# Optimization experiments

Measured on AMD Instinct MI355X. Metric: run time of the kernel, lower is better.

Reference implementation:

```python
import jax, jax.numpy as jnp
import numpy as np

NYRS = 8192
PI = np.pi
MMAX, MMIN = 0.76, 0.01
ALPH, M_TH, MU_TH = 0.093, 4.886, 5.8
ROOTD = 1000.0
I0, IF = 1, 12
M0 = 0.2

NDAYS = np.array([0, 31, 28, 31, 30, 31, 30, 31, 31, 30, 31, 30, 31], dtype=np.float64)
CDAYS = np.cumsum(NDAYS).astype(np.int64)


def _insolation_factors(phi):
    """Static (numpy) day-length factors L[12] and insolation response gE[12].
    phi is a non-differentiated scalar latitude in degrees."""
    latr = phi * PI / 180.0
    jday = np.arange(1, 366, dtype=np.float64)
    sd = np.arcsin(np.sin(PI * 23.5 / 180.0) * np.sin(PI * (jday - 80.0) / 180.0))
    y = np.clip(-np.tan(latr) * np.tan(sd), -1.0, 1.0)
    hdl = np.arccos(y)
    dtsi = hdl * np.sin(latr) * np.sin(sd) + np.cos(latr) * np.cos(sd) * np.sin(hdl)
    ndl = dtsi / dtsi.max()
    jday_mid = CDAYS[:-1] + 0.5 * NDAYS[1:]
    m_star = np.clip(1.0 - np.tan(latr) * np.tan(23.439 * PI / 180.0 * np.cos(jday_mid * PI / 182.625)), 0.0, 2.0)
    nhrs = 24.0 * np.arccos(1.0 - m_star) / PI
    L = NDAYS[1:] / 30.0 * (nhrs / 12.0)  # (12,)
    gE = np.array([ndl[CDAYS[t]:CDAYS[t + 1]].mean() for t in range(12)])  # (12,)
    return L.astype(np.float32), gE.astype(np.float32)


def setup_inputs() -> dict:
    key = jax.random.key(0)
    kT, kP = jax.random.split(key)
    T = 10.0 + 8.0 * jax.random.normal(kT, (NYRS, 12), dtype=jnp.float32)   # degC
    P = 100.0 * jax.random.uniform(kP, (NYRS, 12), dtype=jnp.float32)       # mm/month
    return {
        "syear": 0,
        "eyear": NYRS - 1,
        "phi": 45,
        "T": T,
        "P": P,
        "T1": jnp.float32(8.0),
        "T2": jnp.float32(23.0),
        "M1": jnp.float32(0.01),
        "M2": jnp.float32(0.05),
    }


def reference(syear, eyear, phi, T, P, T1, T2, M1, M2):
    nyrs = eyear - syear + 1
    L_np, gE_np = _insolation_factors(float(phi))
    L = jnp.asarray(L_np)        # (12,)
    gE = jnp.asarray(gE_np)      # (12,)

    Tm = T.T                     # (12, nyrs), month-major like torch code
    Pm = P.T                     # (12, nyrs)

    # ---- potential evapotranspiration (Thornthwaite), vectorized over all months ----
    istar = jnp.maximum(Tm / 5.0, 0.0)
    I = jnp.sum(istar ** 1.514, axis=0)                                   # (nyrs,) heat index
    a = 6.75e-07 * I ** 3 - 7.71e-05 * I ** 2 + 0.0179 * I + 0.49         # (nyrs,)
    Tsafe = jnp.clip(Tm, 0.0, 26.5)                                       # avoid neg-base pow
    Ep_mid = 16.0 * L[:, None] * (10.0 * Tsafe / I[None, :]) ** a[None, :]
    Ep_hot = -415.85 + 32.25 * Tm - 0.43 * Tm ** 2
    potEv = jnp.where(Tm < 0.0, 0.0, jnp.where(Tm < 26.5, Ep_mid, Ep_hot))  # (12, nyrs)

    # ---- leaky-bucket soil-moisture recurrence over the 12*nyrs month chain ----
    Pseq = P.reshape(-1)            # year-major month order (matches M[t,y] chain)
    Epseq = potEv.T.reshape(-1)

    def step(prevM, inp):
        p, ep = inp
        Etrans = ep * prevM * ROOTD / (MMAX * ROOTD)
        G = MU_TH * ALPH / (1.0 + MU_TH) * prevM * ROOTD
        R = p * (prevM * ROOTD / (MMAX * ROOTD)) ** M_TH + ALPH / (1.0 + MU_TH) * prevM * ROOTD
        dWdt = p - Etrans - R - G
        newM = jnp.clip(prevM + dWdt / ROOTD, MMIN, MMAX)
        return newM, newM

    _, Mseq = jax.lax.scan(step, jnp.float32(M0), (Pseq, Epseq))
    M = Mseq.reshape(nyrs, 12).T                                           # (12, nyrs)

    # ---- growth responses ----
    gT = jnp.clip((Tm - T1) / (T2 - T1), 0.0, 1.0)
    gM = jnp.clip((M - M1) / (M2 - M1), 0.0, 1.0)
    Gr = jnp.minimum(gT, gM) * gE[:, None]                                 # (12, nyrs)

    # phi > 0 and I_0 = 1 > 0  ->  width[y] = sum Gr[I0-1:IF, y]
    width = jnp.sum(Gr[I0 - 1:IF, :], axis=0)                              # (nyrs,)
    trw = (width - jnp.mean(width)) / jnp.std(width, ddof=1)               # torch.std is unbiased
    return trw
```

## Files before the change

### kernel.cpp

```cpp
#include <hip/hip_runtime.h>
#include <math.h>

#define PI_F 3.14159265358979323846f
#define WARM_Y 12
#define BY 64
#define BS 64
#define NGRP (BY + WARM_Y)
#define NPAD (NGRP * 13)

#if __has_builtin(__builtin_amdgcn_logf) && __has_builtin(__builtin_amdgcn_exp2f)
__device__ __forceinline__ float flog2(float x) { return __builtin_amdgcn_logf(x); }
__device__ __forceinline__ float fexp2(float x) { return __builtin_amdgcn_exp2f(x); }
#else
__device__ __forceinline__ float flog2(float x) { return log2f(x); }
__device__ __forceinline__ float fexp2(float x) { return exp2f(x); }
#endif
__device__ __forceinline__ float fpow(float x, float y) { return fexp2(y * flog2(x)); }

__constant__ int   c_CDAYS[13]  = {0,31,59,90,120,151,181,212,243,273,304,334,365};
__constant__ float c_NDAYSF[13] = {0,31,28,31,30,31,30,31,31,30,31,30,31};

#define POW_C 1.9345076f

__global__ void k_fused(const int* __restrict__ phi_ptr,
                        const float* __restrict__ T, const float* __restrict__ P,
                        const float* __restrict__ T1p, const float* __restrict__ T2p,
                        const float* __restrict__ M1p, const float* __restrict__ M2p,
                        float* __restrict__ width, int nyrs) {
    __shared__ float sA[NPAD];
    __shared__ float sB[NPAD];
    __shared__ float sT[NPAD];
    __shared__ float dtsi[365];
    __shared__ float sL[12], sGE[12];
    __shared__ float maxd;

    const int tid = threadIdx.x;
    const float latr = (float)(*phi_ptr) * (PI_F / 180.f);
    const float tl = tanf(latr), slat = sinf(latr), clat = cosf(latr);
    const float T1 = *T1p, T2 = *T2p, M1 = *M1p, M2 = *M2p;

    for (int d = tid; d < 365; d += BS) {
        float jd = (float)(d + 1);
        float sd = asinf(sinf(PI_F * 23.5f / 180.f) * sinf(PI_F * (jd - 80.f) / 180.f));
        float y  = fminf(1.f, fmaxf(-1.f, -tl * tanf(sd)));
        float hdl = acosf(y);
        dtsi[d] = hdl * slat * sinf(sd) + clat * cosf(sd) * sinf(hdl);
    }

    const int nmon = nyrs * 12;
    const int base = (blockIdx.x * BY - WARM_Y) * 12;
    for (int t = tid; t < NGRP * 12; t += BS) {
        int tg = base + t;
        int pt = t + t / 12;
        float p = 0.f, tt = 0.f;
        if (tg >= 0 && tg < nmon) { p = P[tg]; tt = T[tg]; }
        sB[pt] = p * 1e-3f;
        sT[pt] = tt;
    }
    __syncthreads();

    {
        float mx = -1e30f;
        for (int i = tid; i < 365; i += BS) mx = fmaxf(mx, dtsi[i]);
        for (int off = 32; off > 0; off >>= 1) mx = fmaxf(mx, __shfl_down(mx, off));
        if (tid == 0) maxd = mx;
    }
    __syncthreads();

    if (tid < 12) {
        int c0 = c_CDAYS[tid], c1 = c_CDAYS[tid + 1];
        float s = 0.f;
        for (int i = c0; i < c1; ++i) s += dtsi[i];
        sGE[tid] = (s / (float)(c1 - c0)) / maxd;
        float nd = c_NDAYSF[tid + 1];
        float jm = (float)c0 + 0.5f * nd;
        float ms = 1.f - tl * tanf(23.439f * PI_F / 180.f * cosf(jm * PI_F / 182.625f));
        ms = fminf(2.f, fmaxf(0.f, ms));
        float nhrs = 24.f * acosf(1.f - ms) / PI_F;
        sL[tid] = nd / 30.f * (nhrs / 12.f);
    }
    __syncthreads();

    for (int g = tid; g < NGRP; g += BS) {
        int yg = blockIdx.x * BY - WARM_Y + g;
        int pt = g * 13;
        if (yg < 0 || yg >= nyrs) {
#pragma unroll
            for (int m = 0; m < 12; ++m) sA[pt + m] = 1.f;
            continue;
        }
        float I = 0.f;
#pragma unroll
        for (int m = 0; m < 12; ++m) {
            float is = fmaxf(sT[pt + m] * 0.2f, 0.f);
            I += fpow(is, 1.514f);
        }
        float a  = 6.75e-07f * I * I * I - 7.71e-05f * I * I + 0.0179f * I + 0.49f;
        float rI = 10.0f / I;
#pragma unroll
        for (int m = 0; m < 12; ++m) {
            float t = sT[pt + m];
            float ep;
            if (t < 0.f)          ep = 0.f;
            else if (t < 26.5f)   ep = 16.f * sL[m] * fpow(t * rI, a);
            else                  ep = -415.85f + 32.25f * t - 0.43f * t * t;
            sA[pt + m] = (1.0f - 0.093f) - ep * (1.0f / 760.0f);
        }
    }
    __syncthreads();

    const int ly = tid;
    const int y = blockIdx.x * BY + ly;
    if (y >= nyrs) return;
    const float invT = 1.0f / (T2 - T1);
    const float invM = 1.0f / (M2 - M1);

    float M = 0.2f;
    int g0 = (blockIdx.x == 0) ? (ly < WARM_Y ? WARM_Y : ly) : ly;

    for (int g = g0; g < ly + WARM_Y; ++g) {
        int pt = g * 13;
#pragma unroll
        for (int m = 0; m < 12; ++m) {
            float a = sA[pt + m], b = sB[pt + m];
            float pw = fexp2(fmaf(4.886f, flog2(M), POW_C));
            float K = fmaf(a, M, b);
            M = fmaf(-b, pw, K);
            M = fminf(0.76f, fmaxf(0.01f, M));
        }
    }
    {
        int pt = (ly + WARM_Y) * 13;
        float acc = 0.f;
#pragma unroll
        for (int m = 0; m < 12; ++m) {
            float a = sA[pt + m], b = sB[pt + m];
            float pw = fexp2(fmaf(4.886f, flog2(M), POW_C));
            float K = fmaf(a, M, b);
            M = fmaf(-b, pw, K);
            M = fminf(0.76f, fmaxf(0.01f, M));
            float gT = fminf(fmaxf((sT[pt + m] - T1) * invT, 0.f), 1.f);
            float gM = fminf(fmaxf((M - M1) * invM, 0.f), 1.f);
            acc += fminf(gT, gM) * sGE[m];
        }
        width[y] = acc;
    }
}

__global__ void k_norm(float* __restrict__ out, int n) {
    __shared__ double s_sum[256];
    __shared__ double s_sq[256];
    __shared__ float mean_s, inv_s;
    const int t = threadIdx.x;
    double sm = 0.0, sq = 0.0;
    for (int i = t; i < n; i += 256) {
        double w = (double)out[i];
        sm += w; sq += w * w;
    }
    s_sum[t] = sm; s_sq[t] = sq;
    __syncthreads();
    for (int off = 128; off > 0; off >>= 1) {
        if (t < off) { s_sum[t] += s_sum[t + off]; s_sq[t] += s_sq[t + off]; }
        __syncthreads();
    }
    if (t == 0) {
        double mean = s_sum[0] / (double)n;
        double var = (s_sq[0] - (double)n * mean * mean) / (double)(n - 1);
        mean_s = (float)mean;
        inv_s = (float)(1.0 / sqrt(var));
    }
    __syncthreads();
    for (int i = t; i < n; i += 256) {
        out[i] = (out[i] - mean_s) * inv_s;
    }
}

extern "C" void kernel_launch(void* const* d_in, const int* in_sizes, int n_in,
                              void* d_out, int out_size, void* d_ws, size_t ws_size,
                              hipStream_t stream) {
    const int*   phi = (const int*)d_in[2];
    const float* T   = (const float*)d_in[3];
    const float* P   = (const float*)d_in[4];
    const float* T1  = (const float*)d_in[5];
    const float* T2  = (const float*)d_in[6];
    const float* M1  = (const float*)d_in[7];
    const float* M2  = (const float*)d_in[8];
    float* out = (float*)d_out;

    const int nyrs = in_sizes[3] / 12;

    k_fused<<<(nyrs + BY - 1) / BY, BS, 0, stream>>>(phi, T, P, T1, T2, M1, M2, out, nyrs);
    k_norm<<<1, 256, 0, stream>>>(out, nyrs);
}
```

Baseline: 98.18 us.

## Fuse normalization into main kernel via last-block reduction of per-block partials

Folds the separate single-block normalization kernel into the main kernel. Each block reduces its widths' sum and sum of squares in double and writes them to a workspace array. An atomic counter picks the last block, which combines the partials and normalizes the whole output. Block size rises to 256 so the setup loops (daylength table, loads) use more threads, while only 64 threads run the recurrence. It removes one kernel launch and the serial re-read of widths, but adds a memset of the counter and relies on threadfence ordering for cross-block visibility.

```diff
diff --git a/kernel.cpp b/kernel.cpp
--- a/kernel.cpp
+++ b/kernel.cpp
@@ -4,7 +4,7 @@
 #define PI_F 3.14159265358979323846f
 #define WARM_Y 12
 #define BY 64
-#define BS 64
+#define BS 256
 #define NGRP (BY + WARM_Y)
 #define NPAD (NGRP * 13)
 
@@ -22,17 +22,19 @@
 
 #define POW_C 1.9345076f
 
-__global__ void k_fused(const int* __restrict__ phi_ptr,
-                        const float* __restrict__ T, const float* __restrict__ P,
-                        const float* __restrict__ T1p, const float* __restrict__ T2p,
-                        const float* __restrict__ M1p, const float* __restrict__ M2p,
-                        float* __restrict__ width, int nyrs) {
+__global__ void k_all(const int* __restrict__ phi_ptr,
+                      const float* __restrict__ T, const float* __restrict__ P,
+                      const float* __restrict__ T1p, const float* __restrict__ T2p,
+                      const float* __restrict__ M1p, const float* __restrict__ M2p,
+                      float* out, unsigned int* ctr, double* partials, int nyrs) {
     __shared__ float sA[NPAD];
     __shared__ float sB[NPAD];
     __shared__ float sT[NPAD];
     __shared__ float dtsi[365];
+    __shared__ float red[BS];
     __shared__ float sL[12], sGE[12];
-    __shared__ float maxd;
+    __shared__ int   is_last_s;
+    __shared__ float mean_s, inv_s;
 
     const int tid = threadIdx.x;
     const float latr = (float)(*phi_ptr) * (PI_F / 180.f);
@@ -62,9 +64,14 @@
     {
         float mx = -1e30f;
         for (int i = tid; i < 365; i += BS) mx = fmaxf(mx, dtsi[i]);
-        for (int off = 32; off > 0; off >>= 1) mx = fmaxf(mx, __shfl_down(mx, off));
-        if (tid == 0) maxd = mx;
-    }
+        red[tid] = mx;
+        __syncthreads();
+        for (int off = BS / 2; off > 0; off >>= 1) {
+            if (tid < off) red[tid] = fmaxf(red[tid], red[tid + off]);
+            __syncthreads();
+        }
+    }
+    const float maxd = red[0];
     __syncthreads();
 
     if (tid < 12) {
@@ -81,96 +88,113 @@
     }
     __syncthreads();
 
-    for (int g = tid; g < NGRP; g += BS) {
+    if (tid < NGRP) {
+        int g = tid;
         int yg = blockIdx.x * BY - WARM_Y + g;
         int pt = g * 13;
         if (yg < 0 || yg >= nyrs) {
 #pragma unroll
             for (int m = 0; m < 12; ++m) sA[pt + m] = 1.f;
-            continue;
-        }
-        float I = 0.f;
-#pragma unroll
-        for (int m = 0; m < 12; ++m) {
-            float is = fmaxf(sT[pt + m] * 0.2f, 0.f);
-            I += fpow(is, 1.514f);
-        }
-        float a  = 6.75e-07f * I * I * I - 7.71e-05f * I * I + 0.0179f * I + 0.49f;
-        float rI = 10.0f / I;
-#pragma unroll
-        for (int m = 0; m < 12; ++m) {
-            float t = sT[pt + m];
-            float ep;
-            if (t < 0.f)          ep = 0.f;
-            else if (t < 26.5f)   ep = 16.f * sL[m] * fpow(t * rI, a);
-            else                  ep = -415.85f + 32.25f * t - 0.43f * t * t;
-            sA[pt + m] = (1.0f - 0.093f) - ep * (1.0f / 760.0f);
-        }
-    }
-    __syncthreads();
-
-    const int ly = tid;
-    const int y = blockIdx.x * BY + ly;
-    if (y >= nyrs) return;
-    const float invT = 1.0f / (T2 - T1);
-    const float invM = 1.0f / (M2 - M1);
-
-    float M = 0.2f;
-    int g0 = (blockIdx.x == 0) ? (ly < WARM_Y ? WARM_Y : ly) : ly;
-
-    for (int g = g0; g < ly + WARM_Y; ++g) {
-        int pt = g * 13;
-#pragma unroll
-        for (int m = 0; m < 12; ++m) {
-            float a = sA[pt + m], b = sB[pt + m];
-            float pw = fexp2(fmaf(4.886f, flog2(M), POW_C));
-            float K = fmaf(a, M, b);
-            M = fmaf(-b, pw, K);
-            M = fminf(0.76f, fmaxf(0.01f, M));
-        }
-    }
-    {
-        int pt = (ly + WARM_Y) * 13;
+        } else {
+            float I = 0.f;
+#pragma unroll
+            for (int m = 0; m < 12; ++m) {
+                float is = fmaxf(sT[pt + m] * 0.2f, 0.f);
+                I += fpow(is, 1.514f);
+            }
+            float a  = 6.75e-07f * I * I * I - 7.71e-05f * I * I + 0.0179f * I + 0.49f;
+            float rI = 10.0f / I;
+#pragma unroll
+            for (int m = 0; m < 12; ++m) {
+                float t = sT[pt + m];
+                float ep;
+                if (t < 0.f)          ep = 0.f;
+                else if (t < 26.5f)   ep = 16.f * sL[m] * fpow(t * rI, a);
+                else                  ep = -415.85f + 32.25f * t - 0.43f * t * t;
+                sA[pt + m] = (1.0f - 0.093f) - ep * (1.0f / 760.0f);
+            }
+        }
+    }
+    __syncthreads();
+
+    double wsum = 0.0, wsq = 0.0;
+    if (tid < BY) {
+        const int ly = tid;
+        const int y = blockIdx.x * BY + ly;
+        const float invT = 1.0f / (T2 - T1);
+        const float invM = 1.0f / (M2 - M1);
+        float M = 0.2f;
+        for (int g = ly; g < ly + WARM_Y; ++g) {
+            int pt = g * 13;
+#pragma unroll
+            for (int m = 0; m < 12; ++m) {
+                float a = sA[pt + m], b = sB[pt + m];
+                float pw = fexp2(fmaf(4.886f, flog2(M), POW_C));
+                float K = fmaf(a, M, b);
+                M = fmaf(-b, pw, K);
+                M = fminf(0.76f, fmaxf(0.01f, M));
+            }
+        }
         float acc = 0.f;
-#pragma unroll
-        for (int m = 0; m < 12; ++m) {
-            float a = sA[pt + m], b = sB[pt + m];
-            float pw = fexp2(fmaf(4.886f, flog2(M), POW_C));
-            float K = fmaf(a, M, b);
-            M = fmaf(-b, pw, K);
-            M = fminf(0.76f, fmaxf(0.01f, M));
-            float gT = fminf(fmaxf((sT[pt + m] - T1) * invT, 0.f), 1.f);
-            float gM = fminf(fmaxf((M - M1) * invM, 0.f), 1.f);
-            acc += fminf(gT, gM) * sGE[m];
-        }
-        width[y] = acc;
-    }
-}
-
-__global__ void k_norm(float* __restrict__ out, int n) {
-    __shared__ double s_sum[256];
-    __shared__ double s_sq[256];
-    __shared__ float mean_s, inv_s;
-    const int t = threadIdx.x;
-    double sm = 0.0, sq = 0.0;
-    for (int i = t; i < n; i += 256) {
-        double w = (double)out[i];
-        sm += w; sq += w * w;
-    }
-    s_sum[t] = sm; s_sq[t] = sq;
-    __syncthreads();
-    for (int off = 128; off > 0; off >>= 1) {
-        if (t < off) { s_sum[t] += s_sum[t + off]; s_sq[t] += s_sq[t + off]; }
-        __syncthreads();
-    }
-    if (t == 0) {
-        double mean = s_sum[0] / (double)n;
-        double var = (s_sq[0] - (double)n * mean * mean) / (double)(n - 1);
-        mean_s = (float)mean;
-        inv_s = (float)(1.0 / sqrt(var));
-    }
-    __syncthreads();
-    for (int i = t; i < n; i += 256) {
+        {
+            int pt = (ly + WARM_Y) * 13;
+#pragma unroll
+            for (int m = 0; m < 12; ++m) {
+                float a = sA[pt + m], b = sB[pt + m];
+                float pw = fexp2(fmaf(4.886f, flog2(M), POW_C));
+                float K = fmaf(a, M, b);
+                M = fmaf(-b, pw, K);
+                M = fminf(0.76f, fmaxf(0.01f, M));
+                float gT = fminf(fmaxf((sT[pt + m] - T1) * invT, 0.f), 1.f);
+                float gM = fminf(fmaxf((M - M1) * invM, 0.f), 1.f);
+                acc += fminf(gT, gM) * sGE[m];
+            }
+        }
+        if (y < nyrs) {
+            out[y] = acc;
+            wsum = (double)acc;
+            wsq  = (double)acc * (double)acc;
+        }
+        for (int off = 32; off > 0; off >>= 1) {
+            wsum += __shfl_down(wsum, off);
+            wsq  += __shfl_down(wsq,  off);
+        }
+        if (ly == 0) {
+            partials[2 * blockIdx.x]     = wsum;
+            partials[2 * blockIdx.x + 1] = wsq;
+        }
+    }
+    __syncthreads();
+
+    if (tid == 0) {
+        __threadfence();
+        unsigned int old = atomicAdd(ctr, 1u);
+        is_last_s = (old == gridDim.x - 1) ? 1 : 0;
+    }
+    __syncthreads();
+    if (!is_last_s) return;
+    __threadfence();
+
+    if (tid < 64) {
+        const int nb = gridDim.x;
+        double sm = 0.0, sq = 0.0;
+        for (int b = tid; b < nb; b += 64) {
+            sm += partials[2 * b];
+            sq += partials[2 * b + 1];
+        }
+        for (int off = 32; off > 0; off >>= 1) {
+            sm += __shfl_down(sm, off);
+            sq += __shfl_down(sq, off);
+        }
+        if (tid == 0) {
+            double mean = sm / (double)nyrs;
+            double var  = (sq - (double)nyrs * mean * mean) / (double)(nyrs - 1);
+            mean_s = (float)mean;
+            inv_s  = (float)(1.0 / sqrt(var));
+        }
+    }
+    __syncthreads();
+    for (int i = tid; i < nyrs; i += BS) {
         out[i] = (out[i] - mean_s) * inv_s;
     }
 }
@@ -188,7 +212,11 @@
     float* out = (float*)d_out;
 
     const int nyrs = in_sizes[3] / 12;
-
-    k_fused<<<(nyrs + BY - 1) / BY, BS, 0, stream>>>(phi, T, P, T1, T2, M1, M2, out, nyrs);
-    k_norm<<<1, 256, 0, stream>>>(out, nyrs);
+    const int nblk = (nyrs + BY - 1) / BY;
+
+    unsigned int* ctr = (unsigned int*)d_ws;
+    double* partials  = (double*)((char*)d_ws + 16);
+
+    hipMemsetAsync(ctr, 0, sizeof(unsigned int), stream);
+    k_all<<<nblk, BS, 0, stream>>>(phi, T, P, T1, T2, M1, M2, out, ctr, partials, nyrs);
 }
```

New measurement: 90.53 us. -7.8%, faster.
